# Kernel tuning notes

Measured on AMD Instinct MI355X. Metric: run time of the kernel, lower is better.

The kernel has to match this reference:

```python
import jax, jax.numpy as jnp
import numpy as np

DEPTH = 4
HEADS = 8
DIM = 512
MLP = 2048
EPS = 1e-5


def layernorm(x, w, b):
    m = x.mean(-1, keepdims=True)
    v = x.var(-1, keepdims=True)
    return (x - m) * jax.lax.rsqrt(v + EPS) * w + b


def setup_inputs() -> dict:
    key = jax.random.key(0)
    ks = jax.random.split(key, 6)
    s = 0.02
    x = jax.random.normal(ks[0], (4, 2048, DIM), dtype=jnp.float32)
    return {
        "x": x,
        "ln1_w": jnp.ones((DEPTH, DIM), jnp.float32),
        "ln1_b": jnp.zeros((DEPTH, DIM), jnp.float32),
        "qkv_w": jax.random.normal(ks[1], (DEPTH, 3 * DIM, DIM), jnp.float32) * s,
        "proj_w": jax.random.normal(ks[2], (DEPTH, DIM, DIM), jnp.float32) * s,
        "proj_b": jnp.zeros((DEPTH, DIM), jnp.float32),
        "ln2_w": jnp.ones((DEPTH, DIM), jnp.float32),
        "ln2_b": jnp.zeros((DEPTH, DIM), jnp.float32),
        "fc1_w": jax.random.normal(ks[3], (DEPTH, MLP, DIM), jnp.float32) * s,
        "fc1_b": jnp.zeros((DEPTH, MLP), jnp.float32),
        "fc2_w": jax.random.normal(ks[4], (DEPTH, DIM, MLP), jnp.float32) * s,
        "fc2_b": jnp.zeros((DEPTH, DIM), jnp.float32),
    }


def reference(x, ln1_w, ln1_b, qkv_w, proj_w, proj_b, ln2_w, ln2_b, fc1_w, fc1_b, fc2_w, fc2_b):
    B, N, C = x.shape
    Dh = C // HEADS
    scale = Dh ** (-0.5)
    for i in range(DEPTH):
        # PreNorm attention block
        h = layernorm(x, ln1_w[i], ln1_b[i])
        qkv = (h @ qkv_w[i].T).reshape(B, N, 3, HEADS, Dh).transpose(2, 0, 3, 1, 4)
        q, k, v = qkv[0], qkv[1], qkv[2]          # [B,H,N,Dh]
        attn = jax.nn.softmax(jnp.einsum('bhnd,bhmd->bhnm', q, k) * scale, axis=-1)
        o = jnp.einsum('bhnm,bhmd->bhnd', attn, v).transpose(0, 2, 1, 3).reshape(B, N, C)
        x = o @ proj_w[i].T + proj_b[i] + x
        # PreNorm FFN block (exact erf GELU, matching torch nn.GELU default)
        h = layernorm(x, ln2_w[i], ln2_b[i])
        h = jax.nn.gelu(h @ fc1_w[i].T + fc1_b[i], approximate=False)
        x = h @ fc2_w[i].T + fc2_b[i] + x
    return x
```

## Files before the change

### kernel.cpp

```cpp
#include <hip/hip_runtime.h>
#include <hip/hip_bf16.h>
#include <math.h>

#define NB 4
#define HEADS 8
#define DIM 512
#define MLP 2048
#define NT 2048
#define DH 64
#define M_TOK (NB*NT)

typedef __bf16 bf16;
typedef __bf16 bf16x2 __attribute__((ext_vector_type(2)));
typedef __bf16 bf16x4 __attribute__((ext_vector_type(4)));
typedef __bf16 bf16x8 __attribute__((ext_vector_type(8)));
typedef float f32x4 __attribute__((ext_vector_type(4)));

__device__ __forceinline__ void gl_lds16(const void* g, void* l) {
    __builtin_amdgcn_global_load_lds((const __attribute__((address_space(1))) unsigned int*)g,
                                     (__attribute__((address_space(3))) unsigned int*)l, 16, 0, 0);
}

#define BARRIER() do { __builtin_amdgcn_s_barrier(); asm volatile("" ::: "memory"); } while(0)
#define WAIT_VM4() asm volatile("s_waitcnt vmcnt(4)" ::: "memory")
#define WAIT_VM0() asm volatile("s_waitcnt vmcnt(0)" ::: "memory")

__global__ void cvt_bf16_kernel(const float* __restrict__ src, bf16* __restrict__ dst, int n) {
    int i = (blockIdx.x * 256 + threadIdx.x) * 4;
    if (i < n) {
        float4 v = *(const float4*)(src + i);
        bf16x4 o;
        o[0] = (bf16)v.x; o[1] = (bf16)v.y; o[2] = (bf16)v.z; o[3] = (bf16)v.w;
        *(bf16x4*)(dst + i) = o;
    }
}

__global__ void ln_kernel(const float* __restrict__ X, const float* __restrict__ gam,
                          const float* __restrict__ bet, bf16* __restrict__ out) {
    int w = threadIdx.x >> 6, l = threadIdx.x & 63;
    long row = (long)blockIdx.x * 4 + w;
    const float* xp = X + row * DIM + l * 8;
    float4 a = *(const float4*)xp;
    float4 b = *(const float4*)(xp + 4);
    float s1 = a.x + a.y + a.z + a.w + b.x + b.y + b.z + b.w;
    float s2 = a.x*a.x + a.y*a.y + a.z*a.z + a.w*a.w + b.x*b.x + b.y*b.y + b.z*b.z + b.w*b.w;
#pragma unroll
    for (int off = 32; off; off >>= 1) { s1 += __shfl_xor(s1, off); s2 += __shfl_xor(s2, off); }
    float mean = s1 * (1.f / 512.f);
    float var  = s2 * (1.f / 512.f) - mean * mean;
    float rstd = rsqrtf(var + 1e-5f);
    float4 g0 = *(const float4*)(gam + l * 8), g1 = *(const float4*)(gam + l * 8 + 4);
    float4 b0 = *(const float4*)(bet + l * 8), b1 = *(const float4*)(bet + l * 8 + 4);
    bf16x8 o;
    o[0] = (bf16)((a.x - mean) * rstd * g0.x + b0.x);
    o[1] = (bf16)((a.y - mean) * rstd * g0.y + b0.y);
    o[2] = (bf16)((a.z - mean) * rstd * g0.z + b0.z);
    o[3] = (bf16)((a.w - mean) * rstd * g0.w + b0.w);
    o[4] = (bf16)((b.x - mean) * rstd * g1.x + b1.x);
    o[5] = (bf16)((b.y - mean) * rstd * g1.y + b1.y);
    o[6] = (bf16)((b.z - mean) * rstd * g1.z + b1.z);
    o[7] = (bf16)((b.w - mean) * rstd * g1.w + b1.w);
    *(bf16x8*)(out + row * DIM + l * 8) = o;
}

#define G_LOADA(AF, B_, MQ) do { \
  _Pragma("unroll") for (int mi_ = 0; mi_ < 2; ++mi_) \
  _Pragma("unroll") for (int kk_ = 0; kk_ < 2; ++kk_) { \
    int row_ = wr * 64 + ((MQ) * 2 + mi_) * 16 + c; \
    AF[mi_][kk_] = *(const bf16x8*)&Abuf[B_][row_ * 64 + (((kk_ * 64 + g * 16) ^ sw) >> 1)]; \
  } } while (0)

#define G_LOADB(BF, B_, NQ) do { \
  _Pragma("unroll") for (int ni_ = 0; ni_ < 2; ++ni_) \
  _Pragma("unroll") for (int kk_ = 0; kk_ < 2; ++kk_) { \
    int row_ = wc * 64 + ((NQ) * 2 + ni_) * 16 + c; \
    BF[ni_][kk_] = *(const bf16x8*)&Bbuf[B_][row_ * 64 + (((kk_ * 64 + g * 16) ^ sw) >> 1)]; \
  } } while (0)

#define G_MFMA(AF, BF, MQ, NQ) do { \
  __builtin_amdgcn_s_setprio(1); \
  _Pragma("unroll") for (int mi_ = 0; mi_ < 2; ++mi_) \
  _Pragma("unroll") for (int ni_ = 0; ni_ < 2; ++ni_) \
  _Pragma("unroll") for (int kk_ = 0; kk_ < 2; ++kk_) \
    acc[(MQ)*2+mi_][(NQ)*2+ni_] = __builtin_amdgcn_mfma_f32_16x16x32_bf16( \
        AF[mi_][kk_], BF[ni_][kk_], acc[(MQ)*2+mi_][(NQ)*2+ni_], 0, 0, 0); \
  __builtin_amdgcn_s_setprio(0); \
} while (0)

#define G_STAGE_A(J_, H_) do { int j_ = (J_); if (j_ < nkt) { \
  bf16* db_ = Abuf[j_ & 1]; const bf16* sb_ = Aptr + (size_t)j_ * 64 + coloff; \
  _Pragma("unroll") for (int q_ = 0; q_ < 2; ++q_) { \
    int rw_ = q_ * 64 + (H_) * 32 + (w << 3); \
    gl_lds16(sb_ + (size_t)(arow0 + rw_ + lr) * KN, db_ + rw_ * 64); \
  } } } while (0)

#define G_STAGE_B(J_, H_) do { int j_ = (J_); if (j_ < nkt) { \
  bf16* db_ = Bbuf[j_ & 1]; const bf16* sb_ = Wptr + (size_t)j_ * 64 + coloff; \
  _Pragma("unroll") for (int q_ = 0; q_ < 2; ++q_) { \
    int rw_ = q_ * 64 + (H_) * 32 + (w << 3); \
    gl_lds16(sb_ + (size_t)(bcol0 + rw_ + lr) * KN, db_ + rw_ * 64); \
  } } } while (0)

template<int EPI, int KN>
__global__ __launch_bounds__(256, 2) void gemm128(const bf16* __restrict__ Aptr,
                                                  const bf16* __restrict__ Wptr,
                                                  const float* __restrict__ bias,
                                                  const float* __restrict__ resid,
                                                  void* outp, int N, bf16* __restrict__ vtout) {
    __shared__ bf16 Abuf[2][128 * 64];
    __shared__ bf16 Bbuf[2][128 * 64];
    const int t = threadIdx.x, w = t >> 6, l = t & 63;
    const int wr = w >> 1, wc = w & 1, g = l >> 4, c = l & 15;
    const int sw = (c & 7) << 4;
    const int lr = l >> 3;
    const int coloff = ((l & 7) ^ lr) << 3;

    int nwg = gridDim.x, bid = blockIdx.x;
    int q8 = nwg >> 3, r8 = nwg & 7;
    int xcd = bid & 7, rank = bid >> 3;
    int swz = (xcd < r8) ? xcd * (q8 + 1) + rank : r8 * (q8 + 1) + (xcd - r8) * q8 + rank;
    int tiles_n = N >> 7;
    long arow0 = (long)(swz / tiles_n) * 128;
    long bcol0 = (long)(swz % tiles_n) * 128;

    const int nkt = KN / 64;
    const int niter = nkt / 2;
    f32x4 acc[4][4] = {};
    bf16x8 af[2][2], bn0[2][2], bn1[2][2];

    G_STAGE_A(0, 0); G_STAGE_B(0, 0); G_STAGE_A(0, 1); G_STAGE_B(0, 1);
    G_STAGE_A(1, 0); G_STAGE_B(1, 0);

#pragma unroll 1
    for (int tt = 0; tt < niter; ++tt) {
        const int J0 = 2 * tt, J1 = 2 * tt + 1;
        const bool last = (tt == niter - 1);
        WAIT_VM4(); BARRIER();
        G_LOADA(af, 0, 0); G_LOADB(bn0, 0, 0);
        G_STAGE_A(J0 + 1, 1);
        G_MFMA(af, bn0, 0, 0);
        BARRIER();
        G_LOADB(bn1, 0, 1);
        G_STAGE_B(J0 + 1, 1);
        G_MFMA(af, bn1, 0, 1);
        BARRIER();
        G_LOADA(af, 0, 1);
        G_STAGE_A(J0 + 2, 0);
        G_MFMA(af, bn0, 1, 0);
        BARRIER();
        G_STAGE_B(J0 + 2, 0);
        G_MFMA(af, bn1, 1, 1);
        BARRIER();
        if (last) { WAIT_VM0(); } else { WAIT_VM4(); }
        BARRIER();
        G_LOADA(af, 1, 0); G_LOADB(bn0, 1, 0);
        G_STAGE_A(J1 + 1, 1);
        G_MFMA(af, bn0, 0, 0);
        BARRIER();
        G_LOADB(bn1, 1, 1);
        G_STAGE_B(J1 + 1, 1);
        G_MFMA(af, bn1, 0, 1);
        BARRIER();
        G_LOADA(af, 1, 1);
        G_STAGE_A(J1 + 2, 0);
        G_MFMA(af, bn0, 1, 0);
        BARRIER();
        G_STAGE_B(J1 + 2, 0);
        G_MFMA(af, bn1, 1, 1);
        BARRIER();
    }

    if constexpr (EPI == 0) {
        const int s = (int)(bcol0 >> 9);
        const float qscale = 0.18033688011112042f;
        if (s == 2) {
#pragma unroll
            for (int m = 0; m < 4; ++m)
#pragma unroll
                for (int n = 0; n < 4; ++n) {
                    int col = (int)(bcol0 + wc * 64 + n * 16 + c);
                    int d = col & 63, hh = (col >> 6) & 7;
                    long row = arow0 + wr * 64 + m * 16 + g * 4;
                    int bb = (int)(row >> 11), nn = (int)(row & 2047);
                    bf16x4 o4;
#pragma unroll
                    for (int r = 0; r < 4; ++r) o4[r] = (bf16)acc[m][n][r];
                    *(bf16x4*)(vtout + ((long)(bb * 8 + hh) * 64 + d) * 2048 + nn) = o4;
                }
        } else {
            const float sc = (s == 0) ? qscale : 1.0f;
#pragma unroll
            for (int m = 0; m < 4; ++m)
#pragma unroll
                for (int n = 0; n < 4; ++n) {
                    int col = (int)(bcol0 + wc * 64 + n * 16 + c);
                    int hh = (col >> 6) & 7, d = col & 63;
                    long row = arow0 + wr * 64 + m * 16 + g * 4;
#pragma unroll
                    for (int r = 0; r < 4; ++r) {
                        long rr = row + r;
                        int bb = (int)(rr >> 11), nn = (int)(rr & 2047);
                        ((bf16*)outp)[(((long)(s * NB + bb) * HEADS + hh) * NT + nn) * DH + d] =
                            (bf16)(acc[m][n][r] * sc);
                    }
                }
        }
    }
}

template<int KN, int NOUT, int EPI>
__global__ __launch_bounds__(256, 2) void gemm_n64(const bf16* __restrict__ A,
                                                   const bf16* __restrict__ W,
                                                   const float* __restrict__ bias,
                                                   const float* __restrict__ resid,
                                                   void* __restrict__ outp) {
    __shared__ bf16 As[128 * 64];
    __shared__ bf16 Bs[64 * 64];
    const int t = threadIdx.x, w = t >> 6, l = t & 63;
    const int wr = w >> 1, wc = w & 1, g = l >> 4, c = l & 15;
    const long arow0 = (long)blockIdx.y * 128;
    const long bcol0 = (long)blockIdx.x * 64;
    f32x4 acc[4][2] = {};
    const int lrow = l >> 3, lcol = (l & 7) * 8;
    const bf16* Ab = A + (arow0 + lrow) * (long)KN + lcol;
    const bf16* Wb = W + (bcol0 + lrow) * (long)KN + lcol;
    for (int k0 = 0; k0 < KN; k0 += 64) {
#pragma unroll
        for (int q = 0; q < 4; ++q)
            gl_lds16(Ab + (long)(w * 4 + q) * 8 * KN + k0, &As[(w * 4 + q) * 512]);
#pragma unroll
        for (int q = 0; q < 2; ++q)
            gl_lds16(Wb + (long)(w * 2 + q) * 8 * KN + k0, &Bs[(w * 2 + q) * 512]);
        __syncthreads();
#pragma unroll
        for (int kk = 0; kk < 2; ++kk) {
            bf16x8 afv[4], bfr[2];
#pragma unroll
            for (int m = 0; m < 4; ++m)
                afv[m] = *(const bf16x8*)&As[(wr * 64 + m * 16 + c) * 64 + kk * 32 + g * 8];
#pragma unroll
            for (int n = 0; n < 2; ++n)
                bfr[n] = *(const bf16x8*)&Bs[(wc * 32 + n * 16 + c) * 64 + kk * 32 + g * 8];
#pragma unroll
            for (int m = 0; m < 4; ++m)
#pragma unroll
                for (int n = 0; n < 2; ++n)
                    acc[m][n] = __builtin_amdgcn_mfma_f32_16x16x32_bf16(afv[m], bfr[n], acc[m][n], 0, 0, 0);
        }
        __syncthreads();
    }
#pragma unroll
    for (int m = 0; m < 4; ++m)
#pragma unroll
        for (int n = 0; n < 2; ++n) {
            long row = arow0 + wr * 64 + m * 16 + g * 4;
            long col = bcol0 + wc * 32 + n * 16 + c;
#pragma unroll
            for (int r = 0; r < 4; ++r) {
                long rr = row + r;
                float v = acc[m][n][r] + bias[col];
                if constexpr (EPI == 1) {
                    ((float*)outp)[rr * NOUT + col] = v + resid[rr * NOUT + col];
                } else {
                    float ge = 0.5f * v * (1.f + erff(v * 0.70710678118654752f));
                    ((bf16*)outp)[rr * NOUT + col] = (bf16)ge;
                }
            }
        }
}

#define NKT (NT / 64)

#define ATT_BODY(BUF, KT) do { \
    __syncthreads(); \
    if ((KT) + 1 < NKT) { \
        const bf16* ks_ = kbase + (size_t)((KT) + 1) * (64 * DH); \
        const bf16* vs_ = vbase + ((KT) + 1) * 64; \
        gl_lds16(ks_,           &Ks[(BUF) ^ 1][(w * 8) * 64]); \
        gl_lds16(ks_ + 32 * DH, &Ks[(BUF) ^ 1][(32 + w * 8) * 64]); \
        gl_lds16(vs_,           &Vs[(BUF) ^ 1][(w * 8) * 64]); \
        gl_lds16(vs_ + 32 * NT, &Vs[(BUF) ^ 1][(32 + w * 8) * 64]); \
    } \
    const bf16* ksb = &Ks[BUF][0]; \
    const char* vsb = (const char*)&Vs[BUF][0]; \
    bf16x8 kf[4][2]; \
    _Pragma("unroll") for (int kc = 0; kc < 4; ++kc) \
    _Pragma("unroll") for (int kk = 0; kk < 2; ++kk) \
        kf[kc][kk] = *(const bf16x8*)&ksb[(kc * 16 + c) * 64 + (((kk * 64 + g * 16) ^ xr) >> 1)]; \
    f32x4 st[4] = {}; \
    _Pragma("unroll") for (int kc = 0; kc < 4; ++kc) \
    _Pragma("unroll") for (int kk = 0; kk < 2; ++kk) \
        st[kc] = __builtin_amdgcn_mfma_f32_16x16x32_bf16(kf[kc][kk], qf[kk], st[kc], 0, 0, 0); \
    bf16x8 vf[4][2]; \
    _Pragma("unroll") for (int dc = 0; dc < 4; ++dc) \
    _Pragma("unroll") for (int ks = 0; ks < 2; ++ks) \
        vf[dc][ks] = *(const bf16x8*)(vsb + (dc * 16 + c) * 128 + ((ks * 64 + g * 16) ^ xr)); \
    bf16x8 pf[2]; \
    _Pragma("unroll") for (int a = 0; a < 4; ++a) \
    _Pragma("unroll") for (int r = 0; r < 4; ++r) \
        pf[a >> 1][(a & 1) * 4 + r] = (bf16)exp2f(st[a][r]); \
    _Pragma("unroll") for (int ks = 0; ks < 2; ++ks) \
        sacc = __builtin_amdgcn_mfma_f32_16x16x32_bf16(ones8, pf[ks], sacc, 0, 0, 0); \
    _Pragma("unroll") for (int dc = 0; dc < 4; ++dc) \
    _Pragma("unroll") for (int ks = 0; ks < 2; ++ks) \
        oacc[dc] = __builtin_amdgcn_mfma_f32_16x16x32_bf16(vf[dc][ks], pf[ks], oacc[dc], 0, 0, 0); \
} while (0)

__global__ __launch_bounds__(256, 4) void attn_kernel(const bf16* __restrict__ qkv,
                                                      const bf16* __restrict__ vt,
                                                      bf16* __restrict__ O) {
    __shared__ bf16 Ks[2][64 * 64];
    __shared__ bf16 Vs[2][64 * 64];
    const int t = threadIdx.x, w = t >> 6, l = t & 63;
    const int g = l >> 4, c = l & 15;
    const int wg = blockIdx.x;
    const int xcd = wg & 7, rank = wg >> 3;
    const int bh = xcd + 8 * (rank >> 5);
    const int qt = rank & 31;
    const bf16* Qb = qkv + (long)bh * (NT * DH);
    const bf16* Kb = Qb + (long)(NB * HEADS) * (NT * DH);
    const bf16* Vtb = vt + (long)bh * (DH * NT);
    const int q0 = qt * 64 + w * 16;
    const int lr = l >> 3, lc = l & 7;
    const int sch = ((lc ^ lr) & 7) * 8;
    const int xr = (c & 7) << 4;

    const bf16* kbase = Kb + (long)(w * 8 + lr) * DH + sch;
    const bf16* vbase = Vtb + (long)(w * 8 + lr) * NT + sch;

    bf16x8 qf[2];
#pragma unroll
    for (int kk = 0; kk < 2; ++kk)
        qf[kk] = *(const bf16x8*)(Qb + (long)(q0 + c) * DH + kk * 32 + g * 8);

    bf16x8 ones8;
#pragma unroll
    for (int j = 0; j < 8; ++j) ones8[j] = (bf16)1.0f;

    f32x4 oacc[4] = {};
    f32x4 sacc = {};

    gl_lds16(kbase,           &Ks[0][(w * 8) * 64]);
    gl_lds16(kbase + 32 * DH, &Ks[0][(32 + w * 8) * 64]);
    gl_lds16(vbase,           &Vs[0][(w * 8) * 64]);
    gl_lds16(vbase + 32 * NT, &Vs[0][(32 + w * 8) * 64]);

#pragma unroll 1
    for (int kt2 = 0; kt2 < NKT / 2; ++kt2) {
        ATT_BODY(0, kt2 * 2);
        ATT_BODY(1, kt2 * 2 + 1);
    }

    float inv = 1.f / sacc[0];

    char* ol = (char*)&Ks[0][0] + w * 2048;
#pragma unroll
    for (int dc = 0; dc < 4; ++dc) {
        bf16x4 o4;
#pragma unroll
        for (int r = 0; r < 4; ++r) o4[r] = (bf16)(oacc[dc][r] * inv);
        *(bf16x4*)(ol + c * 128 + ((dc * 32 + g * 8) ^ xr)) = o4;
    }
    const int orow = l >> 2, oc = (l & 3) * 16;
    const int bb = bh >> 3, hh = bh & 7;
    long tok = (long)bb * NT + q0 + orow;
    bf16* og = O + tok * DIM + hh * 64 + oc;
    const int xr2 = (orow & 7) << 4;
    bf16x8 v0 = *(const bf16x8*)(ol + orow * 128 + ((oc * 2) ^ xr2));
    bf16x8 v1 = *(const bf16x8*)(ol + orow * 128 + ((oc * 2 + 16) ^ xr2));
    *(bf16x8*)og = v0;
    *(bf16x8*)(og + 8) = v1;
}

extern "C" void kernel_launch(void* const* d_in, const int* in_sizes, int n_in,
                              void* d_out, int out_size, void* d_ws, size_t ws_size,
                              hipStream_t stream) {
    const float* x      = (const float*)d_in[0];
    const float* ln1_w  = (const float*)d_in[1];
    const float* ln1_b  = (const float*)d_in[2];
    const float* qkv_w  = (const float*)d_in[3];
    const float* proj_w = (const float*)d_in[4];
    const float* proj_b = (const float*)d_in[5];
    const float* ln2_w  = (const float*)d_in[6];
    const float* ln2_b  = (const float*)d_in[7];
    const float* fc1_w  = (const float*)d_in[8];
    const float* fc1_b  = (const float*)d_in[9];
    const float* fc2_w  = (const float*)d_in[10];
    const float* fc2_b  = (const float*)d_in[11];
    float* X = (float*)d_out;

    char* ws = (char*)d_ws;
    bf16* h_bf   = (bf16*)(ws);
    bf16* scr_bf = (bf16*)(ws + (size_t)(8  << 20));
    bf16* vt_bf  = (bf16*)(ws + (size_t)(32 << 20));
    bf16* o_bf   = (bf16*)(ws + (size_t)(40 << 20));
    bf16* w_qkv  = (bf16*)(ws + (size_t)(48 << 20));
    bf16* w_proj = w_qkv  + (size_t)4 * 1536 * 512;
    bf16* w_fc1  = w_proj + (size_t)4 * 512 * 512;
    bf16* w_fc2  = w_fc1  + (size_t)4 * 2048 * 512;

    {
        int n;
        n = 4 * 1536 * 512; cvt_bf16_kernel<<<n / 1024, 256, 0, stream>>>(qkv_w,  w_qkv,  n);
        n = 4 * 512 * 512;  cvt_bf16_kernel<<<n / 1024, 256, 0, stream>>>(proj_w, w_proj, n);
        n = 4 * 2048 * 512; cvt_bf16_kernel<<<n / 1024, 256, 0, stream>>>(fc1_w,  w_fc1,  n);
        n = 4 * 512 * 2048; cvt_bf16_kernel<<<n / 1024, 256, 0, stream>>>(fc2_w,  w_fc2,  n);
    }
    hipMemcpyAsync(X, x, (size_t)M_TOK * DIM * sizeof(float), hipMemcpyDeviceToDevice, stream);

    for (int i = 0; i < 4; ++i) {
        ln_kernel<<<M_TOK / 4, 256, 0, stream>>>(X, ln1_w + i * 512, ln1_b + i * 512, h_bf);
        gemm128<0, 512><<<(M_TOK / 128) * (1536 / 128), 256, 0, stream>>>(
            h_bf, w_qkv + (size_t)i * 1536 * 512, nullptr, nullptr, scr_bf, 1536, vt_bf);
        attn_kernel<<<1024, 256, 0, stream>>>(scr_bf, vt_bf, o_bf);
        gemm_n64<512, 512, 1><<<dim3(8, 64), 256, 0, stream>>>(
            o_bf, w_proj + (size_t)i * 512 * 512, proj_b + i * 512, X, X);
        ln_kernel<<<M_TOK / 4, 256, 0, stream>>>(X, ln2_w + i * 512, ln2_b + i * 512, h_bf);
        gemm_n64<512, 2048, 2><<<dim3(32, 64), 256, 0, stream>>>(
            h_bf, w_fc1 + (size_t)i * 2048 * 512, fc1_b + i * 2048, nullptr, scr_bf);
        gemm_n64<2048, 512, 1><<<dim3(8, 64), 256, 0, stream>>>(
            scr_bf, w_fc2 + (size_t)i * 512 * 2048, fc2_b + i * 512, X, X);
    }
}
```

Measured before the change: 743.0 us.

## Process two query tiles per attention wave and use 128-wide GEMM for FC1

The attention kernel now has each wave handle 32 query rows (two 16-row MFMA tiles), so each K/V tile loaded into LDS is reused across twice as many queries. The grid is halved and launch bounds drop to 2 blocks per CU to make room for the doubled accumulators. Separately, the FC1+GELU GEMM moves from the 64-wide kernel to the 128x128 gemm128 kernel, via a new GELU epilogue branch. The cost is higher register pressure and fewer resident waves in attention, plus an uncoalesced per-element store in the new epilogue.

```diff
diff --git a/kernel.cpp b/kernel.cpp
--- a/kernel.cpp
+++ b/kernel.cpp
@@ -205,6 +205,21 @@
                     }
                 }
         }
+    } else {
+#pragma unroll
+        for (int m = 0; m < 4; ++m)
+#pragma unroll
+            for (int n = 0; n < 4; ++n) {
+                long row = arow0 + wr * 64 + m * 16 + g * 4;
+                long col = bcol0 + wc * 64 + n * 16 + c;
+#pragma unroll
+                for (int r = 0; r < 4; ++r) {
+                    long rr = row + r;
+                    float u = acc[m][n][r] + bias[col];
+                    float ge = 0.5f * u * (1.f + erff(u * 0.70710678118654752f));
+                    ((bf16*)outp)[rr * N + col] = (bf16)ge;
+                }
+            }
     }
 }
 
@@ -287,26 +302,30 @@
     _Pragma("unroll") for (int kc = 0; kc < 4; ++kc) \
     _Pragma("unroll") for (int kk = 0; kk < 2; ++kk) \
         kf[kc][kk] = *(const bf16x8*)&ksb[(kc * 16 + c) * 64 + (((kk * 64 + g * 16) ^ xr) >> 1)]; \
-    f32x4 st[4] = {}; \
+    f32x4 st[4][2] = {}; \
     _Pragma("unroll") for (int kc = 0; kc < 4; ++kc) \
+    _Pragma("unroll") for (int qi = 0; qi < 2; ++qi) \
     _Pragma("unroll") for (int kk = 0; kk < 2; ++kk) \
-        st[kc] = __builtin_amdgcn_mfma_f32_16x16x32_bf16(kf[kc][kk], qf[kk], st[kc], 0, 0, 0); \
+        st[kc][qi] = __builtin_amdgcn_mfma_f32_16x16x32_bf16(kf[kc][kk], qf[qi][kk], st[kc][qi], 0, 0, 0); \
     bf16x8 vf[4][2]; \
     _Pragma("unroll") for (int dc = 0; dc < 4; ++dc) \
     _Pragma("unroll") for (int ks = 0; ks < 2; ++ks) \
         vf[dc][ks] = *(const bf16x8*)(vsb + (dc * 16 + c) * 128 + ((ks * 64 + g * 16) ^ xr)); \
-    bf16x8 pf[2]; \
+    bf16x8 pf[2][2]; \
+    _Pragma("unroll") for (int qi = 0; qi < 2; ++qi) \
     _Pragma("unroll") for (int a = 0; a < 4; ++a) \
     _Pragma("unroll") for (int r = 0; r < 4; ++r) \
-        pf[a >> 1][(a & 1) * 4 + r] = (bf16)exp2f(st[a][r]); \
+        pf[a >> 1][qi][(a & 1) * 4 + r] = (bf16)exp2f(st[a][qi][r]); \
     _Pragma("unroll") for (int ks = 0; ks < 2; ++ks) \
-        sacc = __builtin_amdgcn_mfma_f32_16x16x32_bf16(ones8, pf[ks], sacc, 0, 0, 0); \
+    _Pragma("unroll") for (int qi = 0; qi < 2; ++qi) \
+        sacc[qi] = __builtin_amdgcn_mfma_f32_16x16x32_bf16(ones8, pf[ks][qi], sacc[qi], 0, 0, 0); \
     _Pragma("unroll") for (int dc = 0; dc < 4; ++dc) \
     _Pragma("unroll") for (int ks = 0; ks < 2; ++ks) \
-        oacc[dc] = __builtin_amdgcn_mfma_f32_16x16x32_bf16(vf[dc][ks], pf[ks], oacc[dc], 0, 0, 0); \
+    _Pragma("unroll") for (int qi = 0; qi < 2; ++qi) \
+        oacc[dc][qi] = __builtin_amdgcn_mfma_f32_16x16x32_bf16(vf[dc][ks], pf[ks][qi], oacc[dc][qi], 0, 0, 0); \
 } while (0)
 
-__global__ __launch_bounds__(256, 4) void attn_kernel(const bf16* __restrict__ qkv,
+__global__ __launch_bounds__(256, 2) void attn_kernel(const bf16* __restrict__ qkv,
                                                       const bf16* __restrict__ vt,
                                                       bf16* __restrict__ O) {
     __shared__ bf16 Ks[2][64 * 64];
@@ -315,12 +334,12 @@
     const int g = l >> 4, c = l & 15;
     const int wg = blockIdx.x;
     const int xcd = wg & 7, rank = wg >> 3;
-    const int bh = xcd + 8 * (rank >> 5);
-    const int qt = rank & 31;
+    const int bh = xcd + 8 * (rank >> 4);
+    const int qt = rank & 15;
     const bf16* Qb = qkv + (long)bh * (NT * DH);
     const bf16* Kb = Qb + (long)(NB * HEADS) * (NT * DH);
     const bf16* Vtb = vt + (long)bh * (DH * NT);
-    const int q0 = qt * 64 + w * 16;
+    const int q0 = qt * 128 + w * 32;
     const int lr = l >> 3, lc = l & 7;
     const int sch = ((lc ^ lr) & 7) * 8;
     const int xr = (c & 7) << 4;
@@ -328,17 +347,19 @@
     const bf16* kbase = Kb + (long)(w * 8 + lr) * DH + sch;
     const bf16* vbase = Vtb + (long)(w * 8 + lr) * NT + sch;
 
-    bf16x8 qf[2];
-#pragma unroll
-    for (int kk = 0; kk < 2; ++kk)
-        qf[kk] = *(const bf16x8*)(Qb + (long)(q0 + c) * DH + kk * 32 + g * 8);
+    bf16x8 qf[2][2];
+#pragma unroll
+    for (int qi = 0; qi < 2; ++qi)
+#pragma unroll
+        for (int kk = 0; kk < 2; ++kk)
+            qf[qi][kk] = *(const bf16x8*)(Qb + (long)(q0 + qi * 16 + c) * DH + kk * 32 + g * 8);
 
     bf16x8 ones8;
 #pragma unroll
     for (int j = 0; j < 8; ++j) ones8[j] = (bf16)1.0f;
 
-    f32x4 oacc[4] = {};
-    f32x4 sacc = {};
+    f32x4 oacc[4][2] = {};
+    f32x4 sacc[2] = {};
 
     gl_lds16(kbase,           &Ks[0][(w * 8) * 64]);
     gl_lds16(kbase + 32 * DH, &Ks[0][(32 + w * 8) * 64]);
@@ -351,25 +372,32 @@
         ATT_BODY(1, kt2 * 2 + 1);
     }
 
-    float inv = 1.f / sacc[0];
-
-    char* ol = (char*)&Ks[0][0] + w * 2048;
-#pragma unroll
-    for (int dc = 0; dc < 4; ++dc) {
-        bf16x4 o4;
-#pragma unroll
-        for (int r = 0; r < 4; ++r) o4[r] = (bf16)(oacc[dc][r] * inv);
-        *(bf16x4*)(ol + c * 128 + ((dc * 32 + g * 8) ^ xr)) = o4;
-    }
     const int orow = l >> 2, oc = (l & 3) * 16;
     const int bb = bh >> 3, hh = bh & 7;
-    long tok = (long)bb * NT + q0 + orow;
-    bf16* og = O + tok * DIM + hh * 64 + oc;
     const int xr2 = (orow & 7) << 4;
-    bf16x8 v0 = *(const bf16x8*)(ol + orow * 128 + ((oc * 2) ^ xr2));
-    bf16x8 v1 = *(const bf16x8*)(ol + orow * 128 + ((oc * 2 + 16) ^ xr2));
-    *(bf16x8*)og = v0;
-    *(bf16x8*)(og + 8) = v1;
+#pragma unroll
+    for (int qi = 0; qi < 2; ++qi) {
+        float inv = 1.f / sacc[qi][0];
+        char* ol = (char*)(qi == 0 ? &Ks[0][0] : &Vs[0][0]) + w * 2048;
+#pragma unroll
+        for (int dc = 0; dc < 4; ++dc) {
+            bf16x4 o4;
+#pragma unroll
+            for (int r = 0; r < 4; ++r) o4[r] = (bf16)(oacc[dc][qi][r] * inv);
+            *(bf16x4*)(ol + c * 128 + ((dc * 32 + g * 8) ^ xr)) = o4;
+        }
+    }
+    __builtin_amdgcn_s_waitcnt(0);
+#pragma unroll
+    for (int qi = 0; qi < 2; ++qi) {
+        const char* ol = (const char*)(qi == 0 ? &Ks[0][0] : &Vs[0][0]) + w * 2048;
+        long tok = (long)bb * NT + q0 + qi * 16 + orow;
+        bf16* og = O + tok * DIM + hh * 64 + oc;
+        bf16x8 v0 = *(const bf16x8*)(ol + orow * 128 + ((oc * 2) ^ xr2));
+        bf16x8 v1 = *(const bf16x8*)(ol + orow * 128 + ((oc * 2 + 16) ^ xr2));
+        *(bf16x8*)og = v0;
+        *(bf16x8*)(og + 8) = v1;
+    }
 }
 
 extern "C" void kernel_launch(void* const* d_in, const int* in_sizes, int n_in,
@@ -412,12 +440,12 @@
         ln_kernel<<<M_TOK / 4, 256, 0, stream>>>(X, ln1_w + i * 512, ln1_b + i * 512, h_bf);
         gemm128<0, 512><<<(M_TOK / 128) * (1536 / 128), 256, 0, stream>>>(
             h_bf, w_qkv + (size_t)i * 1536 * 512, nullptr, nullptr, scr_bf, 1536, vt_bf);
-        attn_kernel<<<1024, 256, 0, stream>>>(scr_bf, vt_bf, o_bf);
+        attn_kernel<<<512, 256, 0, stream>>>(scr_bf, vt_bf, o_bf);
         gemm_n64<512, 512, 1><<<dim3(8, 64), 256, 0, stream>>>(
             o_bf, w_proj + (size_t)i * 512 * 512, proj_b + i * 512, X, X);
         ln_kernel<<<M_TOK / 4, 256, 0, stream>>>(X, ln2_w + i * 512, ln2_b + i * 512, h_bf);
-        gemm_n64<512, 2048, 2><<<dim3(32, 64), 256, 0, stream>>>(
-            h_bf, w_fc1 + (size_t)i * 2048 * 512, fc1_b + i * 2048, nullptr, scr_bf);
+        gemm128<2, 512><<<(M_TOK / 128) * (2048 / 128), 256, 0, stream>>>(
+            h_bf, w_fc1 + (size_t)i * 2048 * 512, fc1_b + i * 2048, nullptr, scr_bf, 2048, nullptr);
         gemm_n64<2048, 512, 1><<<dim3(8, 64), 256, 0, stream>>>(
             scr_bf, w_fc2 + (size_t)i * 512 * 2048, fc2_b + i * 512, X, X);
     }
```

Result: no change. 743.9 us (+0.1%).
